# Performance work log

Hardware: AMD Instinct MI355X
Metric: run time of the kernel (lower is better)

## Reference

```python
import jax, jax.numpy as jnp
import numpy as np

D_IN, D_K, D_V = 1024, 128, 128
B, S = 8, 4096


def setup_inputs() -> dict:
    key = jax.random.key(0)
    kq, kk, kv, kwq, kwk, kwv = jax.random.split(key, 6)
    q = jax.random.normal(kq, (B, S, D_IN), dtype=jnp.float32)
    k = jax.random.normal(kk, (B, S, D_IN), dtype=jnp.float32)
    v = jax.random.normal(kv, (B, S, D_IN), dtype=jnp.float32)
    # nn.Linear(d_in, d_out, bias=None): weight shape [d_out, d_in], y = x @ W^T
    scale = 1.0 / np.sqrt(D_IN)
    Wq = jax.random.uniform(kwq, (D_K, D_IN), jnp.float32, -scale, scale)
    Wk = jax.random.uniform(kwk, (D_K, D_IN), jnp.float32, -scale, scale)
    Wv = jax.random.uniform(kwv, (D_V, D_IN), jnp.float32, -scale, scale)
    return {"q": q, "k": k, "v": v, "Wq": Wq, "Wk": Wk, "Wv": Wv}


def reference(q, k, v, Wq, Wk, Wv):
    # Bias-free projections: [b, s, d_in] @ [d_in, d_k/d_v]
    qh = jnp.einsum('bsd,kd->bsk', q, Wq)
    kh = jnp.einsum('bsd,kd->bsk', k, Wk)
    vh = jnp.einsum('bsd,vd->bsv', v, Wv)
    scores = jnp.einsum('bqk,bsk->bqs', qh, kh) / jnp.sqrt(jnp.float32(D_K))
    attn = jax.nn.softmax(scores, axis=-1)  # [b, s_q, s_kv]
    return jnp.einsum('bqs,bsv->bqv', attn, vh)
```

## Files before the change

kernel.cpp:

```cpp
#include <hip/hip_runtime.h>
#include <hip/hip_bf16.h>
#include <stdint.h>

#define D_IN 1024
#define D_K  128
#define NBATCH 8
#define SEQ  4096
#define MROWS (NBATCH * SEQ)

typedef __attribute__((ext_vector_type(8))) short bf16x8;
typedef __attribute__((ext_vector_type(4))) float f32x4;

__device__ __forceinline__ unsigned short f32_to_bf16(float x) {
    union { float f; uint32_t u; } v; v.f = x;
    uint32_t r = 0x7FFFu + ((v.u >> 16) & 1u);
    return (unsigned short)((v.u + r) >> 16);
}

__device__ __forceinline__ bf16x8 cvt8(float4 lo, float4 hi) {
    bf16x8 r;
    r[0] = (short)f32_to_bf16(lo.x); r[1] = (short)f32_to_bf16(lo.y);
    r[2] = (short)f32_to_bf16(lo.z); r[3] = (short)f32_to_bf16(lo.w);
    r[4] = (short)f32_to_bf16(hi.x); r[5] = (short)f32_to_bf16(hi.y);
    r[6] = (short)f32_to_bf16(hi.z); r[7] = (short)f32_to_bf16(hi.w);
    return r;
}

__device__ __forceinline__ void gload16(const void* src, void* lds) {
    __builtin_amdgcn_global_load_lds(
        (const __attribute__((address_space(1))) void*)src,
        (__attribute__((address_space(3))) void*)lds, 16, 0, 0);
}

__global__ __launch_bounds__(256)
void wconv_kernel(const float* __restrict__ Wq, const float* __restrict__ Wk,
                  const float* __restrict__ Wv, unsigned short* __restrict__ Wt)
{
    const int t  = blockIdx.x * 256 + threadIdx.x;
    const int n  = t & 127;
    const int kc = (t >> 7) & 127;
    const int p  = t >> 14;
    const float* __restrict__ W = (p == 0) ? Wq : (p == 1) ? Wk : Wv;
    const float sc = (p == 0) ? (1.44269504088896f * 0.0883883476483184f) : 1.0f;
    const float4* src = reinterpret_cast<const float4*>(W + (size_t)n * D_IN + kc * 8);
    float4 a = src[0], b = src[1];
    uint4 o;
    o.x = (uint32_t)f32_to_bf16(a.x * sc) | ((uint32_t)f32_to_bf16(a.y * sc) << 16);
    o.y = (uint32_t)f32_to_bf16(a.z * sc) | ((uint32_t)f32_to_bf16(a.w * sc) << 16);
    o.z = (uint32_t)f32_to_bf16(b.x * sc) | ((uint32_t)f32_to_bf16(b.y * sc) << 16);
    o.w = (uint32_t)f32_to_bf16(b.z * sc) | ((uint32_t)f32_to_bf16(b.w * sc) << 16);
    *reinterpret_cast<uint4*>(Wt + (size_t)t * 8) = o;
}

#define RBM 32

__global__ __launch_bounds__(256, 3)
void proj_kernel(const float* __restrict__ Xq, const float* __restrict__ Xk,
                 const float* __restrict__ Xv,
                 const unsigned short* __restrict__ Wt,
                 unsigned short* __restrict__ qh, unsigned short* __restrict__ kh,
                 unsigned short* __restrict__ vhT)
{
    const int p = blockIdx.y;
    const float* __restrict__ X = (p == 0) ? Xq : (p == 1) ? Xk : Xv;
    const unsigned short* __restrict__ Wtp = Wt + (size_t)p * 128 * 128 * 8;

    __shared__ float Asf[RBM * 256];

    const int tid  = threadIdx.x;
    const int lane = tid & 63;
    const int w    = tid >> 6;
    const int lrow = lane & 15;
    const int g    = lane >> 4;
    const int wbase = blockIdx.x * RBM;

    f32x4 acc[2][2];
    #pragma unroll
    for (int mi = 0; mi < 2; ++mi)
        #pragma unroll
        for (int ni = 0; ni < 2; ++ni)
            acc[mi][ni] = (f32x4){0.f, 0.f, 0.f, 0.f};

    char* const abase0 = reinterpret_cast<char*>(Asf) + lrow * 1024;
    char* const abase1 = reinterpret_cast<char*>(Asf) + (16 + lrow) * 1024;
    const int aswz = (lrow & 7) << 5;
    bf16x8 bb[8];

    #pragma unroll
    for (int kk = 0; kk < 4; ++kk) {
        if (kk) __syncthreads();

        const unsigned short* __restrict__ wbk =
            Wtp + ((size_t)(kk * 32 + g) * 128 + w * 32 + lrow) * 8;
        #pragma unroll
        for (int s = 0; s < 4; ++s)
            #pragma unroll
            for (int ni = 0; ni < 2; ++ni)
                bb[s * 2 + ni] = *reinterpret_cast<const bf16x8*>(
                    wbk + ((size_t)(s * 4) * 128 + ni * 16) * 8);

        {
            const int r0 = w * 8;
            const char* src = reinterpret_cast<const char*>(
                X + (size_t)(wbase + r0) * D_IN + kk * 256) + lane * 16;
            float4 L0 = *reinterpret_cast<const float4*>(src);
            float4 L1 = *reinterpret_cast<const float4*>(src + 1 * 4096);
            float4 L2 = *reinterpret_cast<const float4*>(src + 2 * 4096);
            float4 L3 = *reinterpret_cast<const float4*>(src + 3 * 4096);
            float4 L4 = *reinterpret_cast<const float4*>(src + 4 * 4096);
            float4 L5 = *reinterpret_cast<const float4*>(src + 5 * 4096);
            float4 L6 = *reinterpret_cast<const float4*>(src + 6 * 4096);
            float4 L7 = *reinterpret_cast<const float4*>(src + 7 * 4096);
            char* const dst = reinterpret_cast<char*>(Asf);
            const int lb = lane * 16;
            #define WR(i, Li)                                                  \
            do {                                                               \
                const int r_ = r0 + (i);                                       \
                *reinterpret_cast<float4*>(dst + r_ * 1024 +                   \
                    (lb ^ ((r_ & 7) << 5))) = Li;                              \
            } while (0)
            WR(0, L0); WR(1, L1); WR(2, L2); WR(3, L3);
            WR(4, L4); WR(5, L5); WR(6, L6); WR(7, L7);
            #undef WR
        }
        __syncthreads();

        #pragma unroll
        for (int bt = 0; bt < 2; ++bt) {
            #pragma unroll
            for (int s = 0; s < 4; ++s) {
                const int t = bt * 4 + s;
                const int boff = (t * 128 + g * 32) ^ aswz;
                float4 lo0 = *reinterpret_cast<const float4*>(abase0 + boff);
                float4 hi0 = *reinterpret_cast<const float4*>(abase0 + boff + 16);
                float4 lo1 = *reinterpret_cast<const float4*>(abase1 + boff);
                float4 hi1 = *reinterpret_cast<const float4*>(abase1 + boff + 16);
                bf16x8 af0 = cvt8(lo0, hi0);
                bf16x8 af1 = cvt8(lo1, hi1);
                acc[0][0] = __builtin_amdgcn_mfma_f32_16x16x32_bf16(af0, bb[s * 2 + 0], acc[0][0], 0, 0, 0);
                acc[0][1] = __builtin_amdgcn_mfma_f32_16x16x32_bf16(af0, bb[s * 2 + 1], acc[0][1], 0, 0, 0);
                acc[1][0] = __builtin_amdgcn_mfma_f32_16x16x32_bf16(af1, bb[s * 2 + 0], acc[1][0], 0, 0, 0);
                acc[1][1] = __builtin_amdgcn_mfma_f32_16x16x32_bf16(af1, bb[s * 2 + 1], acc[1][1], 0, 0, 0);
                if (bt == 0) {
                    #pragma unroll
                    for (int ni = 0; ni < 2; ++ni)
                        bb[s * 2 + ni] = *reinterpret_cast<const bf16x8*>(
                            wbk + ((size_t)(16 + s * 4) * 128 + ni * 16) * 8);
                }
            }
        }
    }

    if (p < 2) {
        unsigned short* __restrict__ Y = (p == 0) ? qh : kh;
        #pragma unroll
        for (int mi = 0; mi < 2; ++mi) {
            const int rbase = wbase + mi * 16 + g * 4;
            #pragma unroll
            for (int ni = 0; ni < 2; ++ni) {
                const int n = w * 32 + ni * 16 + lrow;
                #pragma unroll
                for (int r = 0; r < 4; ++r)
                    Y[(size_t)(rbase + r) * D_K + n] = f32_to_bf16(acc[mi][ni][r]);
            }
        }
    } else {
        const int b = wbase >> 12;
        #pragma unroll
        for (int mi = 0; mi < 2; ++mi) {
            const int s = (wbase & 4095) + mi * 16 + g * 4;
            #pragma unroll
            for (int ni = 0; ni < 2; ++ni) {
                const int d = w * 32 + ni * 16 + lrow;
                uint2 t;
                t.x = (uint32_t)f32_to_bf16(acc[mi][ni][0]) |
                      ((uint32_t)f32_to_bf16(acc[mi][ni][1]) << 16);
                t.y = (uint32_t)f32_to_bf16(acc[mi][ni][2]) |
                      ((uint32_t)f32_to_bf16(acc[mi][ni][3]) << 16);
                *reinterpret_cast<uint2*>(vhT + ((size_t)(b * D_K + d) << 12) + s) = t;
            }
        }
    }
}

#define KVB 64
#define PSTRIDE 144

__global__ __launch_bounds__(256, 2)
void attn_kernel(const unsigned short* __restrict__ qh,
                 const unsigned short* __restrict__ kh,
                 const unsigned short* __restrict__ vhT,
                 float* __restrict__ out)
{
    __shared__ unsigned short Ks[2][KVB * D_K];
    __shared__ unsigned short Vs[2][D_K * KVB];
    __shared__ char Ps[4][16 * PSTRIDE];

    const int tid  = threadIdx.x;
    const int lane = tid & 63;
    const int wave = tid >> 6;
    const int b    = blockIdx.x & 7;
    const int qt   = blockIdx.x >> 3;
    const int q0   = qt * 64 + wave * 16;
    const int lrow = lane & 15;
    const int g    = lane >> 4;
    const int g4   = g << 2;
    const int lk16 = g * 16;

    const unsigned short* __restrict__ Kb = kh + (size_t)b * SEQ * D_K;
    const unsigned short* __restrict__ Vb = vhT + (size_t)b * D_K * SEQ;
    char* const Pw = Ps[wave];

    const int kr0  = lane >> 4;
    const int kcbp = (lane & 15) * 16;
    const int vr0  = lane >> 3;
    const int vcbp = (lane & 7) * 16;

    #define STAGE(buf, it_)                                                   \
    do {                                                                      \
        const int s0_ = (it_) * KVB;                                          \
        _Pragma("unroll")                                                     \
        for (int j = 0; j < 4; ++j) {                                         \
            const int blk  = wave * 4 + j;                                    \
            const int krow = blk * 4 + kr0;                                   \
            gload16(reinterpret_cast<const char*>(Kb) +                       \
                        (size_t)(s0_ + krow) * 256 +                          \
                        (kcbp ^ ((krow & 7) << 4)),                           \
                    reinterpret_cast<char*>(Ks[buf]) + blk * 1024);           \
            const int vrow = blk * 8 + vr0;                                   \
            gload16(reinterpret_cast<const char*>(Vb) +                       \
                        (size_t)vrow * (SEQ * 2) + (size_t)s0_ * 2 +          \
                        (vcbp ^ ((vrow & 7) << 4)),                           \
                    reinterpret_cast<char*>(Vs[buf]) + blk * 1024);           \
        }                                                                     \
    } while (0)

    bf16x8 qf[4];
    {
        const char* base = reinterpret_cast<const char*>(
            qh + (size_t)(b * SEQ + q0 + lrow) * D_K);
        #pragma unroll
        for (int ks = 0; ks < 4; ++ks)
            qf[ks] = *reinterpret_cast<const bf16x8*>(base + ks * 64 + lk16);
    }

    f32x4 o[8];
    #pragma unroll
    for (int df = 0; df < 8; ++df) o[df] = (f32x4){0.f, 0.f, 0.f, 0.f};
    float lsum = 0.f;

    STAGE(0, 0);
    asm volatile("s_waitcnt vmcnt(0)" ::: "memory");
    __syncthreads();

    int cur = 0;
    for (int it = 0; it < SEQ / KVB; ++it) {
        if (it + 1 < SEQ / KVB) STAGE(cur ^ 1, it + 1);

        f32x4 scT[4];
        #pragma unroll
        for (int sf = 0; sf < 4; ++sf) scT[sf] = (f32x4){0.f, 0.f, 0.f, 0.f};
        #pragma unroll
        for (int ks = 0; ks < 4; ++ks) {
            #pragma unroll
            for (int sf = 0; sf < 4; ++sf) {
                const int row = sf * 16 + lrow;
                bf16x8 kf = *reinterpret_cast<const bf16x8*>(
                    reinterpret_cast<const char*>(Ks[cur]) + row * 256 +
                    ((ks * 64 + lk16) ^ ((row & 7) << 4)));
                scT[sf] = __builtin_amdgcn_mfma_f32_16x16x32_bf16(kf, qf[ks], scT[sf], 0, 0, 0);
            }
        }

        #pragma unroll
        for (int sf = 0; sf < 4; ++sf) {
            float p0 = exp2f(scT[sf][0]);
            float p1 = exp2f(scT[sf][1]);
            float p2 = exp2f(scT[sf][2]);
            float p3 = exp2f(scT[sf][3]);
            lsum += (p0 + p1) + (p2 + p3);
            uint32_t u0, u1;
            asm("v_cvt_pk_bf16_f32 %0, %1, %2" : "=v"(u0) : "v"(p0), "v"(p1));
            asm("v_cvt_pk_bf16_f32 %0, %1, %2" : "=v"(u1) : "v"(p2), "v"(p3));
            uint2 t; t.x = u0; t.y = u1;
            *reinterpret_cast<uint2*>(Pw + lrow * PSTRIDE + (4 * sf + g) * 8) = t;
        }

        #pragma unroll
        for (int ks = 0; ks < 2; ++ks) {
            bf16x8 pf = *reinterpret_cast<const bf16x8*>(
                Pw + lrow * PSTRIDE + ks * 64 + g * 16);
            #pragma unroll
            for (int df = 0; df < 8; ++df) {
                const int vr = df * 16 + lrow;
                bf16x8 vf = *reinterpret_cast<const bf16x8*>(
                    reinterpret_cast<const char*>(Vs[cur]) + vr * 128 +
                    ((ks * 64 + lk16) ^ ((vr & 7) << 4)));
                o[df] = __builtin_amdgcn_mfma_f32_16x16x32_bf16(pf, vf, o[df], 0, 0, 0);
            }
        }

        asm volatile("s_waitcnt vmcnt(0)" ::: "memory");
        __syncthreads();
        cur ^= 1;
    }
    #undef STAGE

    float s = lsum;
    s += __shfl_xor(s, 16);
    s += __shfl_xor(s, 32);
    #pragma unroll
    for (int r = 0; r < 4; ++r) {
        float inv = 1.0f / __shfl(s, g4 + r);
        const int row = q0 + g4 + r;
        float* ob = out + (size_t)(b * SEQ + row) * D_K + lrow;
        #pragma unroll
        for (int df = 0; df < 8; ++df)
            ob[df * 16] = o[df][r] * inv;
    }
}

extern "C" void kernel_launch(void* const* d_in, const int* in_sizes, int n_in,
                              void* d_out, int out_size, void* d_ws, size_t ws_size,
                              hipStream_t stream)
{
    (void)in_sizes; (void)n_in; (void)out_size; (void)ws_size;
    const float* q  = (const float*)d_in[0];
    const float* k  = (const float*)d_in[1];
    const float* v  = (const float*)d_in[2];
    const float* Wq = (const float*)d_in[3];
    const float* Wk = (const float*)d_in[4];
    const float* Wv = (const float*)d_in[5];

    unsigned short* qh  = (unsigned short*)d_ws;
    unsigned short* kh  = qh + (size_t)MROWS * D_K;
    unsigned short* vhT = kh + (size_t)MROWS * D_K;
    unsigned short* Wt  = vhT + (size_t)MROWS * D_K;

    wconv_kernel<<<dim3(192), 256, 0, stream>>>(Wq, Wk, Wv, Wt);
    proj_kernel<<<dim3(MROWS / RBM, 3), 256, 0, stream>>>(q, k, v, Wt, qh, kh, vhT);
    attn_kernel<<<dim3(NBATCH * (SEQ / 64)), 256, 0, stream>>>(qh, kh, vhT, (float*)d_out);
}
```

Before: 205.0 us.

## Double-buffer projection A tiles with direct global-to-LDS loads

The projection kernel now keeps two LDS buffers for the fp32 input tile. It issues direct global-to-LDS loads for the next K-chunk while the MFMAs run on the current one, and the XOR swizzle moves from the LDS store address to the global source address. All 16 weight fragments per K-chunk are preloaded into registers, which removes one barrier per iteration. In exchange, LDS use doubles and launch bounds drop from 3 to 2 blocks per CU, so occupancy falls and register pressure rises.

```diff
diff --git a/kernel.cpp b/kernel.cpp
--- a/kernel.cpp
+++ b/kernel.cpp
@@ -54,7 +54,7 @@
 
 #define RBM 32
 
-__global__ __launch_bounds__(256, 3)
+__global__ __launch_bounds__(256, 2)
 void proj_kernel(const float* __restrict__ Xq, const float* __restrict__ Xk,
                  const float* __restrict__ Xv,
                  const unsigned short* __restrict__ Wt,
@@ -65,7 +65,7 @@
     const float* __restrict__ X = (p == 0) ? Xq : (p == 1) ? Xk : Xv;
     const unsigned short* __restrict__ Wtp = Wt + (size_t)p * 128 * 128 * 8;
 
-    __shared__ float Asf[RBM * 256];
+    __shared__ float Asf[2][RBM * 256];
 
     const int tid  = threadIdx.x;
     const int lane = tid & 63;
@@ -73,6 +73,7 @@
     const int lrow = lane & 15;
     const int g    = lane >> 4;
     const int wbase = blockIdx.x * RBM;
+    const char* __restrict__ Xb = reinterpret_cast<const char*>(X);
 
     f32x4 acc[2][2];
     #pragma unroll
@@ -81,75 +82,62 @@
         for (int ni = 0; ni < 2; ++ni)
             acc[mi][ni] = (f32x4){0.f, 0.f, 0.f, 0.f};
 
-    char* const abase0 = reinterpret_cast<char*>(Asf) + lrow * 1024;
-    char* const abase1 = reinterpret_cast<char*>(Asf) + (16 + lrow) * 1024;
     const int aswz = (lrow & 7) << 5;
-    bf16x8 bb[8];
-
+    bf16x8 bb[16];
+
+    #define STAGE_A(buf, kk_)                                                 \
+    do {                                                                      \
+        _Pragma("unroll")                                                     \
+        for (int i = 0; i < 8; ++i) {                                         \
+            const int r_ = w * 8 + i;                                         \
+            gload16(Xb + (size_t)(wbase + r_) * 4096 + (kk_) * 1024 +         \
+                        ((lane * 16) ^ ((r_ & 7) << 5)),                      \
+                    reinterpret_cast<char*>(Asf[buf]) + r_ * 1024);           \
+        }                                                                     \
+    } while (0)
+
+    STAGE_A(0, 0);
+    asm volatile("s_waitcnt vmcnt(0)" ::: "memory");
+    __syncthreads();
+
+    int buf = 0;
     #pragma unroll
     for (int kk = 0; kk < 4; ++kk) {
-        if (kk) __syncthreads();
-
         const unsigned short* __restrict__ wbk =
             Wtp + ((size_t)(kk * 32 + g) * 128 + w * 32 + lrow) * 8;
         #pragma unroll
-        for (int s = 0; s < 4; ++s)
+        for (int t = 0; t < 8; ++t)
             #pragma unroll
             for (int ni = 0; ni < 2; ++ni)
-                bb[s * 2 + ni] = *reinterpret_cast<const bf16x8*>(
-                    wbk + ((size_t)(s * 4) * 128 + ni * 16) * 8);
-
-        {
-            const int r0 = w * 8;
-            const char* src = reinterpret_cast<const char*>(
-                X + (size_t)(wbase + r0) * D_IN + kk * 256) + lane * 16;
-            float4 L0 = *reinterpret_cast<const float4*>(src);
-            float4 L1 = *reinterpret_cast<const float4*>(src + 1 * 4096);
-            float4 L2 = *reinterpret_cast<const float4*>(src + 2 * 4096);
-            float4 L3 = *reinterpret_cast<const float4*>(src + 3 * 4096);
-            float4 L4 = *reinterpret_cast<const float4*>(src + 4 * 4096);
-            float4 L5 = *reinterpret_cast<const float4*>(src + 5 * 4096);
-            float4 L6 = *reinterpret_cast<const float4*>(src + 6 * 4096);
-            float4 L7 = *reinterpret_cast<const float4*>(src + 7 * 4096);
-            char* const dst = reinterpret_cast<char*>(Asf);
-            const int lb = lane * 16;
-            #define WR(i, Li)                                                  \
-            do {                                                               \
-                const int r_ = r0 + (i);                                       \
-                *reinterpret_cast<float4*>(dst + r_ * 1024 +                   \
-                    (lb ^ ((r_ & 7) << 5))) = Li;                              \
-            } while (0)
-            WR(0, L0); WR(1, L1); WR(2, L2); WR(3, L3);
-            WR(4, L4); WR(5, L5); WR(6, L6); WR(7, L7);
-            #undef WR
-        }
-        __syncthreads();
-
-        #pragma unroll
-        for (int bt = 0; bt < 2; ++bt) {
-            #pragma unroll
-            for (int s = 0; s < 4; ++s) {
-                const int t = bt * 4 + s;
-                const int boff = (t * 128 + g * 32) ^ aswz;
-                float4 lo0 = *reinterpret_cast<const float4*>(abase0 + boff);
-                float4 hi0 = *reinterpret_cast<const float4*>(abase0 + boff + 16);
-                float4 lo1 = *reinterpret_cast<const float4*>(abase1 + boff);
-                float4 hi1 = *reinterpret_cast<const float4*>(abase1 + boff + 16);
-                bf16x8 af0 = cvt8(lo0, hi0);
-                bf16x8 af1 = cvt8(lo1, hi1);
-                acc[0][0] = __builtin_amdgcn_mfma_f32_16x16x32_bf16(af0, bb[s * 2 + 0], acc[0][0], 0, 0, 0);
-                acc[0][1] = __builtin_amdgcn_mfma_f32_16x16x32_bf16(af0, bb[s * 2 + 1], acc[0][1], 0, 0, 0);
-                acc[1][0] = __builtin_amdgcn_mfma_f32_16x16x32_bf16(af1, bb[s * 2 + 0], acc[1][0], 0, 0, 0);
-                acc[1][1] = __builtin_amdgcn_mfma_f32_16x16x32_bf16(af1, bb[s * 2 + 1], acc[1][1], 0, 0, 0);
-                if (bt == 0) {
-                    #pragma unroll
-                    for (int ni = 0; ni < 2; ++ni)
-                        bb[s * 2 + ni] = *reinterpret_cast<const bf16x8*>(
-                            wbk + ((size_t)(16 + s * 4) * 128 + ni * 16) * 8);
-                }
-            }
-        }
-    }
+                bb[t * 2 + ni] = *reinterpret_cast<const bf16x8*>(
+                    wbk + ((size_t)(t * 4) * 128 + ni * 16) * 8);
+
+        if (kk < 3) STAGE_A(buf ^ 1, kk + 1);
+
+        const char* const base = reinterpret_cast<const char*>(Asf[buf]);
+        const char* const a0 = base + lrow * 1024;
+        const char* const a1 = base + (16 + lrow) * 1024;
+        #pragma unroll
+        for (int t = 0; t < 8; ++t) {
+            const int boff = (t * 128 + g * 32) ^ aswz;
+            float4 lo0 = *reinterpret_cast<const float4*>(a0 + boff);
+            float4 hi0 = *reinterpret_cast<const float4*>(a0 + boff + 16);
+            float4 lo1 = *reinterpret_cast<const float4*>(a1 + boff);
+            float4 hi1 = *reinterpret_cast<const float4*>(a1 + boff + 16);
+            bf16x8 af0 = cvt8(lo0, hi0);
+            bf16x8 af1 = cvt8(lo1, hi1);
+            acc[0][0] = __builtin_amdgcn_mfma_f32_16x16x32_bf16(af0, bb[t * 2 + 0], acc[0][0], 0, 0, 0);
+            acc[0][1] = __builtin_amdgcn_mfma_f32_16x16x32_bf16(af0, bb[t * 2 + 1], acc[0][1], 0, 0, 0);
+            acc[1][0] = __builtin_amdgcn_mfma_f32_16x16x32_bf16(af1, bb[t * 2 + 0], acc[1][0], 0, 0, 0);
+            acc[1][1] = __builtin_amdgcn_mfma_f32_16x16x32_bf16(af1, bb[t * 2 + 1], acc[1][1], 0, 0, 0);
+        }
+
+        if (kk < 3) {
+            __syncthreads();
+            buf ^= 1;
+        }
+    }
+    #undef STAGE_A
 
     if (p < 2) {
         unsigned short* __restrict__ Y = (p == 0) ? qh : kh;
```

After: 235.0 us. 1.15x slower.
